# Kernel tuning notes

Hardware: AMD Instinct MI355X
Metric: run time of the kernel (lower is better)

The kernel has to match this reference:

```python
import jax, jax.numpy as jnp
import numpy as np

N_NODES = 100000
N_EDGES = 1600000
NFEAT = 128
NHID = 64  # layer widths: NFEAT -> 2*NHID -> NHID


def gcn_conv(x, edge_index, edge_weight, W, b):
    """PyG GCNConv: add self-loops, symmetric D^-1/2 (A+I) D^-1/2 normalization."""
    n = x.shape[0]
    h = x @ W  # [N, out]
    src = edge_index[0]
    dst = edge_index[1]
    # degree at destination including self-loop weight 1
    deg = jax.ops.segment_sum(edge_weight, dst, num_segments=n) + 1.0
    dinv = jax.lax.rsqrt(deg)  # deg >= 1, always finite
    norm = dinv[src] * edge_weight * dinv[dst]  # [E]
    agg = jax.ops.segment_sum(h[src] * norm[:, None], dst, num_segments=n)
    agg = agg + h * (dinv * dinv)[:, None]  # self-loop contribution: 1/deg
    return agg + b


def setup_inputs() -> dict:
    key = jax.random.key(0)
    k1, k2, k3, k4, k5, k6 = jax.random.split(key, 6)
    x = jax.random.normal(k1, (N_NODES, NFEAT), dtype=jnp.float32)
    edge_index = jax.random.randint(k2, (2, N_EDGES), 0, N_NODES, dtype=jnp.int64)
    edge_weight = jnp.ones((N_EDGES,), dtype=jnp.float32)
    # GCNConv weights (glorot-ish scale)
    W1 = jax.random.normal(k3, (NFEAT, 2 * NHID), dtype=jnp.float32) / np.sqrt(NFEAT)
    b1 = jnp.zeros((2 * NHID,), dtype=jnp.float32)
    W2 = jax.random.normal(k4, (2 * NHID, NHID), dtype=jnp.float32) / np.sqrt(2 * NHID)
    b2 = jnp.zeros((NHID,), dtype=jnp.float32)
    return {"x": x, "edge_index": edge_index, "edge_weight": edge_weight,
            "W1": W1, "b1": b1, "W2": W2, "b2": b2}


def reference(x, edge_index, edge_weight, W1, b1, W2, b2):
    # GCN_body forward, eval mode (dropout = identity, use_ln/layer_norm_first = False)
    h = jax.nn.relu(gcn_conv(x, edge_index, edge_weight, W1, b1))
    h = jax.nn.relu(gcn_conv(h, edge_index, edge_weight, W2, b2))
    return h
```

## Files before the change

### kernel.cpp

```cpp
#include <hip/hip_runtime.h>

static constexpr int NN = 100000;
static constexpr int NE = 1600000;
static constexpr int BK = 391;
static constexpr int BK2 = 392;
static constexpr int BCAP = 4864;
static constexpr int NBA = 512;
static constexpr int PCAP = 32;
static constexpr int CHUNK = NE / NBA;

typedef _Float16 f16x8 __attribute__((ext_vector_type(8)));
typedef float f32x4 __attribute__((ext_vector_type(4)));

__global__ __launch_bounds__(512) void binA_kernel(const int* __restrict__ src,
                                                   const int* __restrict__ dst,
                                                   const float* __restrict__ w,
                                                   int* __restrict__ cnts,
                                                   long long* __restrict__ binned) {
  __shared__ int hist[BK2];
  __shared__ int localoff[BK2];
  __shared__ int wsum[4];
  __shared__ unsigned long long ebuf[CHUNK];
  __shared__ unsigned short bkts[CHUNK];
  const int t = threadIdx.x;
  const int blk = blockIdx.x;
  const int e0 = blk * CHUNK;
  const int e1 = e0 + CHUNK;

  for (int i = t; i < BK2; i += 512) hist[i] = 0;
  __syncthreads();
  for (int e = e0 + t; e < e1; e += 512) atomicAdd(&hist[dst[e] >> 8], 1);
  __syncthreads();
  for (int i = t; i < BK; i += 512) cnts[i * NBA + blk] = min(hist[i], PCAP);

  int h0 = 0, h1 = 0, c = 0;
  if (t < 196) {
    h0 = hist[2 * t];
    h1 = hist[2 * t + 1];
    c = h0 + h1;
  }
  if (t < 256) {
    const int lane = t & 63;
    int incl = c;
#pragma unroll
    for (int d2 = 1; d2 < 64; d2 <<= 1) {
      int v2 = __shfl_up(incl, d2, 64);
      if (lane >= d2) incl += v2;
    }
    if (lane == 63) wsum[t >> 6] = incl;
    __syncthreads();
    int wbase = 0;
#pragma unroll
    for (int ww = 0; ww < 4; ++ww) wbase += (ww < (t >> 6)) ? wsum[ww] : 0;
    if (t < 196) {
      int ex = wbase + incl - c;
      localoff[2 * t] = ex;
      localoff[2 * t + 1] = ex + h0;
    }
  } else {
    __syncthreads();
  }
  __syncthreads();
  for (int i = t; i < BK2; i += 512) hist[i] = 0;
  __syncthreads();

  for (int e = e0 + t; e < e1; e += 512) {
    int d = dst[e];
    int bkt = d >> 8;
    int slot = atomicAdd(&hist[bkt], 1);
    int pos = localoff[bkt] + slot;
    unsigned lo = (unsigned)src[e] | ((unsigned)(d & 255) << 20);
    ebuf[pos] = ((unsigned long long)__float_as_uint(w[e]) << 32) | lo;
    bkts[pos] = (unsigned short)bkt;
  }
  __syncthreads();

  for (int pos = t; pos < CHUNK; pos += 512) {
    int bkt = bkts[pos];
    int slot = pos - localoff[bkt];
    if (slot < PCAP)
      binned[((size_t)bkt * NBA + blk) * PCAP + slot] = (long long)ebuf[pos];
  }
}

__global__ __launch_bounds__(256) void buildB_kernel(const int* __restrict__ cnts,
                                                     long long* __restrict__ binned,
                                                     int2* __restrict__ meta,
                                                     float* __restrict__ dinv) {
  __shared__ long long eb[BCAP];
  __shared__ int scnt[NBA];
  __shared__ int segbase[NBA];
  __shared__ int cnt[256];
  __shared__ int off[256];
  __shared__ int cur[256];
  __shared__ float degs[256];
  __shared__ int wsum[4];
  __shared__ int tot_s;
  const int b = blockIdx.x;
  const int t = threadIdx.x;
  long long* gb = binned + (size_t)b * NBA * PCAP;

  scnt[t] = cnts[b * NBA + t];
  scnt[t + 256] = cnts[b * NBA + t + 256];
  __syncthreads();

  {
    int s0 = scnt[2 * t];
    int s1 = scnt[2 * t + 1];
    int c2 = s0 + s1;
    const int lane = t & 63;
    int incl = c2;
#pragma unroll
    for (int d2 = 1; d2 < 64; d2 <<= 1) {
      int v2 = __shfl_up(incl, d2, 64);
      if (lane >= d2) incl += v2;
    }
    if (lane == 63) wsum[t >> 6] = incl;
    __syncthreads();
    int wbase = 0;
#pragma unroll
    for (int ww = 0; ww < 4; ++ww) wbase += (ww < (t >> 6)) ? wsum[ww] : 0;
    int ex = wbase + incl - c2;
    segbase[2 * t] = ex;
    segbase[2 * t + 1] = ex + s0;
    if (t == 255) tot_s = ex + c2;
  }
  __syncthreads();
  const int m = min(tot_s, BCAP);

  {
    const int wv = t >> 6;
    const int lane = t & 63;
    for (int p = wv; p < NBA / 2; p += 4) {
      int s = 2 * p + (lane >> 5);
      int i = lane & 31;
      if (i < scnt[s]) {
        int db = segbase[s] + i;
        if (db < BCAP) eb[db] = gb[(size_t)s * PCAP + i];
      }
    }
  }
  cnt[t] = 0;
  degs[t] = 0.f;
  __syncthreads();

  for (int i = t; i < m; i += 256) {
    unsigned long long v = (unsigned long long)eb[i];
    int dl = (int)((v >> 20) & 255u);
    atomicAdd(&cnt[dl], 1);
    atomicAdd(&degs[dl], __uint_as_float((unsigned)(v >> 32)));
  }
  __syncthreads();

  const int lane = t & 63;
  const int c = cnt[t];
  int incl = c;
#pragma unroll
  for (int d2 = 1; d2 < 64; d2 <<= 1) {
    int v2 = __shfl_up(incl, d2, 64);
    if (lane >= d2) incl += v2;
  }
  if (lane == 63) wsum[t >> 6] = incl;
  __syncthreads();
  int wbase = 0;
#pragma unroll
  for (int ww = 0; ww < 4; ++ww) wbase += (ww < (t >> 6)) ? wsum[ww] : 0;
  const int myoff = wbase + incl - c;
  off[t] = myoff;
  cur[t] = 0;
  __syncthreads();

  for (int i = t; i < m; i += 256) {
    long long v = eb[i];
    int dl = (int)(((unsigned long long)v >> 20) & 255u);
    int slot = atomicAdd(&cur[dl], 1);
    gb[off[dl] + slot] = v;
  }

  const int n = b * 256 + t;
  if (n < NN) {
    meta[n] = make_int2(b * NBA * PCAP + myoff, c);
    dinv[n] = rsqrtf(degs[t] + 1.0f);
  }
}

__global__ void wfrag_kernel(const float* __restrict__ W1, const float* __restrict__ W2,
                             _Float16* __restrict__ wf1, _Float16* __restrict__ wf2) {
  int i = blockIdx.x * blockDim.x + threadIdx.x;
  const float* W;
  _Float16* wf;
  int N, idx;
  if (i < 128 * 128) {
    W = W1; wf = wf1; N = 128; idx = i;
  } else if (i < 128 * 128 + 64 * 128) {
    W = W2; wf = wf2; N = 64; idx = i - 128 * 128;
  } else return;
  int j = idx & 7;
  int l = (idx >> 3) & 63;
  int ks = (idx >> 9) & 3;
  int t = idx >> 11;
  int n = t * 16 + (l & 15);
  int k = ks * 32 + (l >> 4) * 8 + j;
  wf[idx] = (_Float16)W[k * N + n];
}

template <int N, typename AT>
__global__ __launch_bounds__(256) void mfma_gemm_kernel(const AT* __restrict__ X,
                                                        const _Float16* __restrict__ wf,
                                                        _Float16* __restrict__ H) {
  constexpr int NT = N / 16;
  const int w = threadIdx.x >> 6;
  const int l = threadIdx.x & 63;
  const int row0 = (blockIdx.x * 4 + w) * 16;
  const int arow = row0 + (l & 15);
  const int kb = (l >> 4) * 8;

  f16x8 a[4];
  if (arow < NN) {
    const AT* xp = X + (size_t)arow * 128 + kb;
#pragma unroll
    for (int ks = 0; ks < 4; ++ks) {
      if constexpr (sizeof(AT) == 4) {
        float4 lo = *(const float4*)(xp + ks * 32);
        float4 hi = *(const float4*)(xp + ks * 32 + 4);
        f16x8 v;
        v[0] = (_Float16)lo.x; v[1] = (_Float16)lo.y;
        v[2] = (_Float16)lo.z; v[3] = (_Float16)lo.w;
        v[4] = (_Float16)hi.x; v[5] = (_Float16)hi.y;
        v[6] = (_Float16)hi.z; v[7] = (_Float16)hi.w;
        a[ks] = v;
      } else {
        a[ks] = *(const f16x8*)(xp + ks * 32);
      }
    }
  } else {
    f16x8 z;
#pragma unroll
    for (int j = 0; j < 8; ++j) z[j] = (_Float16)0.f;
#pragma unroll
    for (int ks = 0; ks < 4; ++ks) a[ks] = z;
  }

  f32x4 acc[NT];
#pragma unroll
  for (int t = 0; t < NT; ++t) acc[t] = {0.f, 0.f, 0.f, 0.f};

  const _Float16* wp = wf + l * 8;
#pragma unroll
  for (int t = 0; t < NT; ++t) {
#pragma unroll
    for (int ks = 0; ks < 4; ++ks) {
      f16x8 b = *(const f16x8*)(wp + (size_t)(t * 4 + ks) * 512);
      acc[t] = __builtin_amdgcn_mfma_f32_16x16x32_f16(a[ks], b, acc[t], 0, 0, 0);
    }
  }

  const int r0 = row0 + (l >> 4) * 4;
  const int c0 = l & 15;
#pragma unroll
  for (int t = 0; t < NT; ++t) {
#pragma unroll
    for (int r = 0; r < 4; ++r) {
      int row = r0 + r;
      if (row < NN) H[(size_t)row * N + t * 16 + c0] = (_Float16)acc[t][r];
    }
  }
}

template <int F, typename OT>
__global__ __launch_bounds__(256) void gather_kernel(
    const int2* __restrict__ meta, const long long* __restrict__ csr,
    const _Float16* __restrict__ H, const float* __restrict__ dinv,
    const float* __restrict__ b, OT* __restrict__ out) {
  constexpr int TPN = F / 8;
  constexpr int NPB = 256 / TPN;
  const int t = threadIdx.x;
  const int node = blockIdx.x * NPB + t / TPN;
  if (node >= NN) return;
  const int g = t % TPN;
  const int f = g * 8;

  const int2 mt = meta[node];
  const int lo = mt.x;
  const int cnt = mt.y;
  const float di = dinv[node];
  const float sl = di * di;

  f16x8 hs = *(const f16x8*)(H + (size_t)node * F + f);
  float c[8], aA[8], aB[8];
#pragma unroll
  for (int j = 0; j < 8; ++j) {
    c[j] = fmaf((float)hs[j], sl, b[f + j]);
    aA[j] = 0.f;
    aB[j] = 0.f;
  }

  for (int base = 0; base < cnt; base += TPN) {
    const int rem = cnt - base;
    const int m = rem < TPN ? rem : TPN;
    int idx = base + (g < m ? g : m - 1);
    unsigned long long ce = (unsigned long long)csr[lo + idx];
    int s_l = (int)(ce & 0x1FFFFu);
    float nrm_l = dinv[s_l] * __uint_as_float((unsigned)(ce >> 32));

    int e = 0;
    for (; e + 1 < m; e += 2) {
      int s0 = __shfl(s_l, e, TPN);
      float n0 = __shfl(nrm_l, e, TPN);
      int s1 = __shfl(s_l, e + 1, TPN);
      float n1 = __shfl(nrm_l, e + 1, TPN);
      f16x8 h0 = *(const f16x8*)(H + (size_t)s0 * F + f);
      f16x8 h1 = *(const f16x8*)(H + (size_t)s1 * F + f);
#pragma unroll
      for (int j = 0; j < 8; ++j) {
        aA[j] = fmaf((float)h0[j], n0, aA[j]);
        aB[j] = fmaf((float)h1[j], n1, aB[j]);
      }
    }
    if (e < m) {
      int s0 = __shfl(s_l, e, TPN);
      float n0 = __shfl(nrm_l, e, TPN);
      f16x8 h0 = *(const f16x8*)(H + (size_t)s0 * F + f);
#pragma unroll
      for (int j = 0; j < 8; ++j) aA[j] = fmaf((float)h0[j], n0, aA[j]);
    }
  }

  float o[8];
#pragma unroll
  for (int j = 0; j < 8; ++j) o[j] = fmaxf(fmaf(aA[j] + aB[j], di, c[j]), 0.f);

  if constexpr (sizeof(OT) == 2) {
    f16x8 v;
#pragma unroll
    for (int j = 0; j < 8; ++j) v[j] = (_Float16)o[j];
    *(f16x8*)(out + (size_t)node * F + f) = v;
  } else {
    float4 v0 = make_float4(o[0], o[1], o[2], o[3]);
    float4 v1 = make_float4(o[4], o[5], o[6], o[7]);
    *(float4*)(out + (size_t)node * F + f) = v0;
    *(float4*)(out + (size_t)node * F + f + 4) = v1;
  }
}

extern "C" void kernel_launch(void* const* d_in, const int* in_sizes, int n_in,
                              void* d_out, int out_size, void* d_ws, size_t ws_size,
                              hipStream_t stream) {
  const float* x  = (const float*)d_in[0];
  const int*   ei = (const int*)d_in[1];
  const float* ew = (const float*)d_in[2];
  const float* W1 = (const float*)d_in[3];
  const float* b1 = (const float*)d_in[4];
  const float* W2 = (const float*)d_in[5];
  const float* b2 = (const float*)d_in[6];
  float* out = (float*)d_out;

  const int* src = ei;
  const int* dst = ei + NE;

  float* wsf        = (float*)d_ws;
  int*   cnts       = (int*)wsf;
  float* dinv       = wsf + BK * NBA;
  int2*  meta       = (int2*)(dinv + NN);
  long long* binned = (long long*)(meta + NN);
  float* fbase      = (float*)(binned + (size_t)BK * NBA * PCAP);
  _Float16* h1      = (_Float16*)fbase;
  _Float16* a1      = (_Float16*)(fbase + (size_t)NN * 64);
  _Float16* wf1     = (_Float16*)(fbase + (size_t)NN * 128);
  _Float16* wf2     = wf1 + 16384;
  _Float16* h2      = h1;

  binA_kernel<<<NBA, 512, 0, stream>>>(src, dst, ew, cnts, binned);
  buildB_kernel<<<BK, 256, 0, stream>>>(cnts, binned, meta, dinv);
  wfrag_kernel<<<96, 256, 0, stream>>>(W1, W2, wf1, wf2);

  mfma_gemm_kernel<128, float><<<(NN + 63) / 64, 256, 0, stream>>>(x, wf1, h1);
  gather_kernel<128, _Float16><<<(NN * 16 + 255) / 256, 256, 0, stream>>>(meta, binned,
                                                                          h1, dinv, b1, a1);

  mfma_gemm_kernel<64, _Float16><<<(NN + 63) / 64, 256, 0, stream>>>(a1, wf2, h2);
  gather_kernel<64, float><<<(NN * 8 + 255) / 256, 256, 0, stream>>>(meta, binned,
                                                                     h2, dinv, b2, out);
}
```

Measured before the change: 195.0 us.

## Fuse layer-1 aggregation with layer-2 GEMM and simplify edge loop

```diff
diff --git a/kernel.cpp b/kernel.cpp
--- a/kernel.cpp
+++ b/kernel.cpp
@@ -267,26 +267,26 @@
   }
 }
 
-template <int F, typename OT>
-__global__ __launch_bounds__(256) void gather_kernel(
+__global__ __launch_bounds__(256) void gather_gemm_kernel(
     const int2* __restrict__ meta, const long long* __restrict__ csr,
     const _Float16* __restrict__ H, const float* __restrict__ dinv,
-    const float* __restrict__ b, OT* __restrict__ out) {
-  constexpr int TPN = F / 8;
-  constexpr int NPB = 256 / TPN;
+    const float* __restrict__ b, const _Float16* __restrict__ wf2,
+    _Float16* __restrict__ h2) {
+  constexpr int LDA = 136;
+  __shared__ _Float16 als[16 * LDA];
   const int t = threadIdx.x;
-  const int node = blockIdx.x * NPB + t / TPN;
-  if (node >= NN) return;
-  const int g = t % TPN;
+  const int nl = t >> 4;
+  const int node = blockIdx.x * 16 + nl;
+  const int g = t & 15;
   const int f = g * 8;
 
   const int2 mt = meta[node];
   const int lo = mt.x;
-  const int cnt = mt.y;
+  const int hi = mt.x + mt.y;
   const float di = dinv[node];
   const float sl = di * di;
 
-  f16x8 hs = *(const f16x8*)(H + (size_t)node * F + f);
+  f16x8 hs = *(const f16x8*)(H + (size_t)node * 128 + f);
   float c[8], aA[8], aB[8];
 #pragma unroll
   for (int j = 0; j < 8; ++j) {
@@ -295,52 +295,115 @@
     aB[j] = 0.f;
   }
 
-  for (int base = 0; base < cnt; base += TPN) {
-    const int rem = cnt - base;
-    const int m = rem < TPN ? rem : TPN;
-    int idx = base + (g < m ? g : m - 1);
-    unsigned long long ce = (unsigned long long)csr[lo + idx];
-    int s_l = (int)(ce & 0x1FFFFu);
-    float nrm_l = dinv[s_l] * __uint_as_float((unsigned)(ce >> 32));
-
-    int e = 0;
-    for (; e + 1 < m; e += 2) {
-      int s0 = __shfl(s_l, e, TPN);
-      float n0 = __shfl(nrm_l, e, TPN);
-      int s1 = __shfl(s_l, e + 1, TPN);
-      float n1 = __shfl(nrm_l, e + 1, TPN);
-      f16x8 h0 = *(const f16x8*)(H + (size_t)s0 * F + f);
-      f16x8 h1 = *(const f16x8*)(H + (size_t)s1 * F + f);
-#pragma unroll
-      for (int j = 0; j < 8; ++j) {
-        aA[j] = fmaf((float)h0[j], n0, aA[j]);
-        aB[j] = fmaf((float)h1[j], n1, aB[j]);
-      }
-    }
-    if (e < m) {
-      int s0 = __shfl(s_l, e, TPN);
-      float n0 = __shfl(nrm_l, e, TPN);
-      f16x8 h0 = *(const f16x8*)(H + (size_t)s0 * F + f);
-#pragma unroll
-      for (int j = 0; j < 8; ++j) aA[j] = fmaf((float)h0[j], n0, aA[j]);
-    }
-  }
-
-  float o[8];
-#pragma unroll
-  for (int j = 0; j < 8; ++j) o[j] = fmaxf(fmaf(aA[j] + aB[j], di, c[j]), 0.f);
-
-  if constexpr (sizeof(OT) == 2) {
-    f16x8 v;
-#pragma unroll
-    for (int j = 0; j < 8; ++j) v[j] = (_Float16)o[j];
-    *(f16x8*)(out + (size_t)node * F + f) = v;
-  } else {
-    float4 v0 = make_float4(o[0], o[1], o[2], o[3]);
-    float4 v1 = make_float4(o[4], o[5], o[6], o[7]);
-    *(float4*)(out + (size_t)node * F + f) = v0;
-    *(float4*)(out + (size_t)node * F + f + 4) = v1;
-  }
+  int i = lo;
+  for (; i + 1 < hi; i += 2) {
+    unsigned long long v0 = (unsigned long long)csr[i];
+    unsigned long long v1 = (unsigned long long)csr[i + 1];
+    int s0 = (int)(v0 & 0x1FFFFu);
+    int s1 = (int)(v1 & 0x1FFFFu);
+    float n0 = dinv[s0] * __uint_as_float((unsigned)(v0 >> 32));
+    float n1 = dinv[s1] * __uint_as_float((unsigned)(v1 >> 32));
+    f16x8 h0 = *(const f16x8*)(H + (size_t)s0 * 128 + f);
+    f16x8 h1 = *(const f16x8*)(H + (size_t)s1 * 128 + f);
+#pragma unroll
+    for (int j = 0; j < 8; ++j) {
+      aA[j] = fmaf((float)h0[j], n0, aA[j]);
+      aB[j] = fmaf((float)h1[j], n1, aB[j]);
+    }
+  }
+  if (i < hi) {
+    unsigned long long v0 = (unsigned long long)csr[i];
+    int s0 = (int)(v0 & 0x1FFFFu);
+    float n0 = dinv[s0] * __uint_as_float((unsigned)(v0 >> 32));
+    f16x8 h0 = *(const f16x8*)(H + (size_t)s0 * 128 + f);
+#pragma unroll
+    for (int j = 0; j < 8; ++j) aA[j] = fmaf((float)h0[j], n0, aA[j]);
+  }
+
+  f16x8 av;
+#pragma unroll
+  for (int j = 0; j < 8; ++j)
+    av[j] = (_Float16)fmaxf(fmaf(aA[j] + aB[j], di, c[j]), 0.f);
+  *(f16x8*)(als + nl * LDA + f) = av;
+  __syncthreads();
+
+  const int w = t >> 6;
+  const int l = t & 63;
+  f32x4 acc = {0.f, 0.f, 0.f, 0.f};
+  const _Float16* ap = als + (l & 15) * LDA + (l >> 4) * 8;
+  const _Float16* wp = wf2 + (size_t)w * 4 * 512 + l * 8;
+#pragma unroll
+  for (int ks = 0; ks < 4; ++ks) {
+    f16x8 afrag = *(const f16x8*)(ap + ks * 32);
+    f16x8 bfrag = *(const f16x8*)(wp + ks * 512);
+    acc = __builtin_amdgcn_mfma_f32_16x16x32_f16(afrag, bfrag, acc, 0, 0, 0);
+  }
+  const int orow = blockIdx.x * 16 + (l >> 4) * 4;
+  const int ocol = w * 16 + (l & 15);
+#pragma unroll
+  for (int r = 0; r < 4; ++r)
+    h2[(size_t)(orow + r) * 64 + ocol] = (_Float16)acc[r];
+}
+
+__global__ __launch_bounds__(256) void gather64_kernel(
+    const int2* __restrict__ meta, const long long* __restrict__ csr,
+    const _Float16* __restrict__ H, const float* __restrict__ dinv,
+    const float* __restrict__ b, float* __restrict__ out) {
+  const int t = threadIdx.x;
+  const int node = blockIdx.x * 32 + (t >> 3);
+  const int f = (t & 7) * 8;
+
+  const int2 mt = meta[node];
+  const int lo = mt.x;
+  const int hi = mt.x + mt.y;
+  const float di = dinv[node];
+  const float sl = di * di;
+
+  f16x8 hs = *(const f16x8*)(H + (size_t)node * 64 + f);
+  float c[8], aA[8], aB[8];
+#pragma unroll
+  for (int j = 0; j < 8; ++j) {
+    c[j] = fmaf((float)hs[j], sl, b[f + j]);
+    aA[j] = 0.f;
+    aB[j] = 0.f;
+  }
+
+  int i = lo;
+  for (; i + 1 < hi; i += 2) {
+    unsigned long long v0 = (unsigned long long)csr[i];
+    unsigned long long v1 = (unsigned long long)csr[i + 1];
+    int s0 = (int)(v0 & 0x1FFFFu);
+    int s1 = (int)(v1 & 0x1FFFFu);
+    float n0 = dinv[s0] * __uint_as_float((unsigned)(v0 >> 32));
+    float n1 = dinv[s1] * __uint_as_float((unsigned)(v1 >> 32));
+    f16x8 h0 = *(const f16x8*)(H + (size_t)s0 * 64 + f);
+    f16x8 h1 = *(const f16x8*)(H + (size_t)s1 * 64 + f);
+#pragma unroll
+    for (int j = 0; j < 8; ++j) {
+      aA[j] = fmaf((float)h0[j], n0, aA[j]);
+      aB[j] = fmaf((float)h1[j], n1, aB[j]);
+    }
+  }
+  if (i < hi) {
+    unsigned long long v0 = (unsigned long long)csr[i];
+    int s0 = (int)(v0 & 0x1FFFFu);
+    float n0 = dinv[s0] * __uint_as_float((unsigned)(v0 >> 32));
+    f16x8 h0 = *(const f16x8*)(H + (size_t)s0 * 64 + f);
+#pragma unroll
+    for (int j = 0; j < 8; ++j) aA[j] = fmaf((float)h0[j], n0, aA[j]);
+  }
+
+  float4 v0, v1;
+  v0.x = fmaxf(fmaf(aA[0] + aB[0], di, c[0]), 0.f);
+  v0.y = fmaxf(fmaf(aA[1] + aB[1], di, c[1]), 0.f);
+  v0.z = fmaxf(fmaf(aA[2] + aB[2], di, c[2]), 0.f);
+  v0.w = fmaxf(fmaf(aA[3] + aB[3], di, c[3]), 0.f);
+  v1.x = fmaxf(fmaf(aA[4] + aB[4], di, c[4]), 0.f);
+  v1.y = fmaxf(fmaf(aA[5] + aB[5], di, c[5]), 0.f);
+  v1.z = fmaxf(fmaf(aA[6] + aB[6], di, c[6]), 0.f);
+  v1.w = fmaxf(fmaf(aA[7] + aB[7], di, c[7]), 0.f);
+  *(float4*)(out + (size_t)node * 64 + f) = v0;
+  *(float4*)(out + (size_t)node * 64 + f + 4) = v1;
 }
 
 extern "C" void kernel_launch(void* const* d_in, const int* in_sizes, int n_in,
@@ -365,20 +428,15 @@
   long long* binned = (long long*)(meta + NN);
   float* fbase      = (float*)(binned + (size_t)BK * NBA * PCAP);
   _Float16* h1      = (_Float16*)fbase;
-  _Float16* a1      = (_Float16*)(fbase + (size_t)NN * 64);
-  _Float16* wf1     = (_Float16*)(fbase + (size_t)NN * 128);
+  _Float16* h2      = (_Float16*)(fbase + (size_t)NN * 64);
+  _Float16* wf1     = (_Float16*)(fbase + (size_t)NN * 96);
   _Float16* wf2     = wf1 + 16384;
-  _Float16* h2      = h1;
 
   binA_kernel<<<NBA, 512, 0, stream>>>(src, dst, ew, cnts, binned);
   buildB_kernel<<<BK, 256, 0, stream>>>(cnts, binned, meta, dinv);
   wfrag_kernel<<<96, 256, 0, stream>>>(W1, W2, wf1, wf2);
 
   mfma_gemm_kernel<128, float><<<(NN + 63) / 64, 256, 0, stream>>>(x, wf1, h1);
-  gather_kernel<128, _Float16><<<(NN * 16 + 255) / 256, 256, 0, stream>>>(meta, binned,
-                                                                          h1, dinv, b1, a1);
-
-  mfma_gemm_kernel<64, _Float16><<<(NN + 63) / 64, 256, 0, stream>>>(a1, wf2, h2);
-  gather_kernel<64, float><<<(NN * 8 + 255) / 256, 256, 0, stream>>>(meta, binned,
-                                                                     h2, dinv, b2, out);
-}
+  gather_gemm_kernel<<<NN / 16, 256, 0, stream>>>(meta, binned, h1, dinv, b1, wf2, h2);
+  gather64_kernel<<<NN / 32, 256, 0, stream>>>(meta, binned, h2, dinv, b2, out);
+}
```

Result: faster. 185.7 us (-4.8%).
